# Kernel optimization log

Measured on AMD Instinct MI355X. Metric: run time of the kernel, lower is better.

## Reference

```python
import jax, jax.numpy as jnp
import numpy as np
from jax.ops import segment_sum, segment_max

N_NODES, N_EDGES, D_IN, D_H, D_E, HEADS, LAYERS, D_OUT, N_GRAPHS = 50000, 150000, 48, 64, 16, 10, 3, 128, 4096


def setup_inputs() -> dict:
    key = jax.random.key(0)
    ks = jax.random.split(key, 24)
    x = jax.random.normal(ks[0], (N_NODES, D_IN), jnp.float32)
    edge_attr = jax.random.uniform(ks[1], (N_EDGES, D_E), jnp.float32)
    edge_index = jax.random.randint(ks[2], (2, N_EDGES), 0, N_NODES, dtype=jnp.int32)
    batch_ids = jnp.sort(jax.random.randint(ks[3], (N_NODES,), 0, N_GRAPHS, dtype=jnp.int32))
    s = 0.05
    W_emb = jax.random.normal(ks[4], (D_IN, D_H), jnp.float32) * s
    b_emb = jnp.zeros((D_H,), jnp.float32)
    Ws = jax.random.normal(ks[5], (LAYERS, D_H, HEADS * D_H), jnp.float32) * s
    att_src = jax.random.normal(ks[6], (LAYERS, HEADS, D_H), jnp.float32) * s
    att_dst = jax.random.normal(ks[7], (LAYERS, HEADS, D_H), jnp.float32) * s
    att_edge = jax.random.normal(ks[8], (LAYERS, HEADS, D_H), jnp.float32) * s
    W_edge = jax.random.normal(ks[9], (LAYERS, D_E, HEADS * D_H), jnp.float32) * s
    bias = jnp.zeros((LAYERS, D_H), jnp.float32)
    bn_gamma = jnp.ones((LAYERS, D_H), jnp.float32)
    bn_beta = jnp.zeros((LAYERS, D_H), jnp.float32)
    bn_mean = jax.random.normal(ks[10], (LAYERS, D_H), jnp.float32) * 0.1
    bn_var = jax.random.uniform(ks[11], (LAYERS, D_H), jnp.float32) + 0.5
    W_out = jax.random.normal(ks[12], (D_H, D_OUT), jnp.float32) * s
    b_out = jnp.zeros((D_OUT,), jnp.float32)
    return dict(x=x, edge_attr=edge_attr, W_emb=W_emb, b_emb=b_emb, Ws=Ws,
                att_src=att_src, att_dst=att_dst, att_edge=att_edge, W_edge=W_edge,
                bias=bias, bn_gamma=bn_gamma, bn_beta=bn_beta, bn_mean=bn_mean,
                bn_var=bn_var, W_out=W_out, b_out=b_out,
                edge_index=edge_index, batch_ids=batch_ids)


def reference(x, edge_attr, W_emb, b_emb, Ws, att_src, att_dst, att_edge, W_edge,
              bias, bn_gamma, bn_beta, bn_mean, bn_var, W_out, b_out,
              edge_index, batch_ids):
    N = x.shape[0]
    H, F = att_src.shape[1], att_src.shape[2]
    src, dst = edge_index[0], edge_index[1]
    # PyG add_self_loops(fill_value='mean'): self-loop edge_attr = scatter-mean of incoming edge_attr
    cnt = segment_sum(jnp.ones(src.shape, jnp.float32), dst, num_segments=N)
    loop_attr = segment_sum(edge_attr, dst, num_segments=N) / jnp.maximum(cnt, 1.0)[:, None]
    ar = jnp.arange(N, dtype=src.dtype)
    src2 = jnp.concatenate([src, ar])
    dst2 = jnp.concatenate([dst, ar])
    ea2 = jnp.concatenate([edge_attr, loop_attr], axis=0)  # [E+N, De]

    h = x @ W_emb + b_emb  # [N, D_H]
    for i in range(Ws.shape[0]):
        xp = (h @ Ws[i]).reshape(N, H, F)                       # [N,H,F]
        a_s = jnp.einsum('nhf,hf->nh', xp, att_src[i])
        a_d = jnp.einsum('nhf,hf->nh', xp, att_dst[i])
        ep = (ea2 @ W_edge[i]).reshape(-1, H, F)                # [E2,H,F]
        a_e = jnp.einsum('ehf,hf->eh', ep, att_edge[i])
        alpha = jax.nn.leaky_relu(a_s[src2] + a_d[dst2] + a_e, 0.2)  # [E2,H]
        m = segment_max(alpha, dst2, num_segments=N)            # segment softmax over dst
        e = jnp.exp(alpha - m[dst2])
        z = segment_sum(e, dst2, num_segments=N)
        att = e / z[dst2]                                       # [E2,H]
        agg = segment_sum(xp[src2] * att[:, :, None], dst2, num_segments=N)  # [N,H,F]
        xc = agg.mean(axis=1) + bias[i]                         # concat=False -> head mean
        xc = (xc - bn_mean[i]) * bn_gamma[i] / jnp.sqrt(bn_var[i] + 1e-5) + bn_beta[i]
        xc = jax.nn.gelu(xc, approximate=False)
        h = h + xc                                              # residual_connection == 'res'
    out = h @ W_out + b_out                                     # [N, D_OUT]
    gsum = segment_sum(out, batch_ids, num_segments=N_GRAPHS)
    gcnt = segment_sum(jnp.ones((N,), jnp.float32), batch_ids, num_segments=N_GRAPHS)
    return gsum / jnp.maximum(gcnt, 1.0)[:, None]               # global_mean_pool [G, D_OUT]
```

## Files before the change

### kernel.cpp

```cpp
#include <hip/hip_runtime.h>
#include <hip/hip_fp16.h>
#include <math.h>

constexpr int NN   = 50000;
constexpr int NE   = 150000;
constexpr int DIN  = 48;
constexpr int DH   = 64;
constexpr int DE   = 16;
constexpr int NHD  = 10;
constexpr int NL   = 3;
constexpr int DOUTC= 128;
constexpr int NG   = 4096;
constexpr int E2   = NE + NN;
constexpr int SCAN_B  = 256;
constexpr int SCAN_NB = (NN + SCAN_B - 1) / SCAN_B;

typedef __bf16 v8bf __attribute__((ext_vector_type(8)));
typedef short  v8s  __attribute__((ext_vector_type(8)));
typedef float  v4f  __attribute__((ext_vector_type(4)));

__device__ inline unsigned short f2bf(float f) {
    unsigned u = __builtin_bit_cast(unsigned, f);
    unsigned r = (u + 0x7FFFu + ((u >> 16) & 1u)) >> 16;
    return (unsigned short)r;
}

__device__ inline v4f MF(v8s a, v8s b, v4f c) {
    return __builtin_amdgcn_mfma_f32_16x16x32_bf16(
        __builtin_bit_cast(v8bf, a), __builtin_bit_cast(v8bf, b), c, 0, 0, 0);
}
__device__ inline v4f MFB(v8bf a, v8s b, v4f c) {
    return __builtin_amdgcn_mfma_f32_16x16x32_bf16(
        a, __builtin_bit_cast(v8bf, b), c, 0, 0, 0);
}

#define RLI(v, l) __builtin_amdgcn_readlane((v), (l))
#define RLH2(v, l) __builtin_bit_cast(__half2, __builtin_amdgcn_readlane(__builtin_bit_cast(int, (v)), (l)))

__global__ void k_cnt(const int* __restrict__ dst, int* __restrict__ cnt) {
    int e = blockIdx.x * blockDim.x + threadIdx.x;
    if (e < NE) atomicAdd(&cnt[dst[e]], 1);
}

__global__ void k_scan_a(const int* __restrict__ cnt, int* __restrict__ bsum) {
    __shared__ int s[SCAN_B];
    int i = blockIdx.x * SCAN_B + threadIdx.x;
    s[threadIdx.x] = (i < NN) ? (cnt[i] + 1) : 0;
    __syncthreads();
    for (int off = SCAN_B / 2; off > 0; off >>= 1) {
        if (threadIdx.x < off) s[threadIdx.x] += s[threadIdx.x + off];
        __syncthreads();
    }
    if (threadIdx.x == 0) bsum[blockIdx.x] = s[0];
}

__global__ void k_scan_c(const int* __restrict__ cnt, const int* __restrict__ bsum,
                         int* __restrict__ rp, int* __restrict__ cursor) {
    __shared__ int s[SCAN_B];
    __shared__ int boff_s;
    const int t = threadIdx.x;
    int partial = (t < SCAN_NB && t < blockIdx.x) ? bsum[t] : 0;
    s[t] = partial;
    __syncthreads();
    for (int off = SCAN_B / 2; off > 0; off >>= 1) {
        if (t < off) s[t] += s[t + off];
        __syncthreads();
    }
    if (t == 0) boff_s = s[0];
    __syncthreads();
    const int boff = boff_s;
    __syncthreads();
    int i = blockIdx.x * SCAN_B + t;
    if (i < NN) cursor[i] = 0;
    int v = (i < NN) ? (cnt[i] + 1) : 0;
    s[t] = v;
    __syncthreads();
    for (int off = 1; off < SCAN_B; off <<= 1) {
        int tv = (t >= off) ? s[t - off] : 0;
        __syncthreads();
        s[t] += tv;
        __syncthreads();
    }
    if (i < NN) {
        int excl = boff + s[t] - v;
        rp[i] = excl;
        if (i == NN - 1) rp[NN] = excl + v;
    }
}

__global__ void k_csr_fill(const int* __restrict__ src, const int* __restrict__ dst,
                           const int* __restrict__ rp, int* __restrict__ cursor,
                           int* __restrict__ eidx, int* __restrict__ scsr) {
    int e = blockIdx.x * blockDim.x + threadIdx.x;
    if (e >= E2) return;
    int d  = (e < NE) ? dst[e] : (e - NE);
    int sn = (e < NE) ? src[e] : d;
    int pos = atomicAdd(&cursor[d], 1);
    int s = rp[d] + pos;
    eidx[s] = e; scsr[s] = sn;
}

__global__ void k_misc(const int* __restrict__ rp, const int* __restrict__ scsr,
                       const int* __restrict__ eidx, const int* __restrict__ cnt,
                       const float* __restrict__ ea, const int* __restrict__ batch,
                       int* __restrict__ snl12, int* __restrict__ grp,
                       float* __restrict__ loop) {
    int tid = blockIdx.x * blockDim.x + threadIdx.x;
    if (tid < NN * 16) {
        int n = tid >> 4, j = tid & 15;
        int r0 = rp[n], deg = rp[n + 1] - r0;
        int v;
        if (j < 12)      v = (j < deg) ? scsr[r0 + j] : 0;
        else if (j == 12) v = deg;
        else if (j == 13) v = r0;
        else             v = 0;
        snl12[tid] = v;
    } else if (tid < NN * 17) {
        int n = tid - NN * 16;
        int b = batch[n];
        int pb = (n == 0) ? -1 : batch[n - 1];
        for (int g = pb + 1; g <= b; ++g) grp[g] = n;
        if (n == NN - 1) for (int g = b + 1; g <= NG; ++g) grp[g] = NN;
    } else if (tid < NN * 33) {
        int t = tid - NN * 17;
        int n = t >> 4, d = t & 15;
        int r0 = rp[n], r1 = rp[n + 1];
        float s = 0.f;
        for (int q = r0; q < r1; ++q) {
            int eid = eidx[q];
            if (eid < NE) s += ea[(size_t)eid * DE + d];
        }
        int c = cnt[n];
        loop[t] = s * ((c > 1) ? (1.0f / (float)c) : 1.0f);
    }
}

constexpr int N_BTP = NL * 40960;
constexpr int N_WCB = NL * 2048;
constexpr int N_EMB = DH * 64;
constexpr int N_WET = NL * DE * NHD;
constexpr int N_PRE = N_BTP + N_WCB + N_EMB + N_WET + NN;
__global__ void k_prep(const float* __restrict__ Ws, const float* __restrict__ asrc,
                       const float* __restrict__ adst, const float* __restrict__ We_in,
                       const float* __restrict__ aedge, const float* __restrict__ Wemb,
                       unsigned short* __restrict__ BtP, unsigned short* __restrict__ WcB,
                       unsigned short* __restrict__ BH, unsigned short* __restrict__ BL,
                       float* __restrict__ WeT, int* __restrict__ cnt) {
    int tid = blockIdx.x * blockDim.x + threadIdx.x;
    if (tid < N_BTP) {
        int e  = tid & 7;
        int ln = (tid >> 3) & 63;
        int t  = (tid >> 9) % 20;
        int ct = (tid / 10240) & 3;
        int l  = tid / 40960;
        int f = ct * 16 + (ln & 15);
        int kidx = t * 32 + (ln >> 4) * 8 + e;
        int k = kidx / 10, q = kidx - 10 * (kidx / 10);
        float v = Ws[((size_t)l * DH + k) * 640 + q * 64 + f] * 0.1f;
        BtP[tid] = f2bf(v);
    } else if (tid < N_BTP + N_WCB) {
        int r0 = tid - N_BTP;
        int l = r0 / 2048, r = r0 % 2048;
        int tile = r / 1024, rr = r % 1024;
        int ln = rr / 16, idx = rr % 16;
        int t2 = idx / 8, e = idx % 8;
        int k = t2 * 32 + (ln >> 4) * 8 + e;
        int jc = ln & 15;
        int j = tile * 16 + jc;
        float v = 0.f;
        if (j < 20) {
            int hh = j % NHD;
            const float* a = ((j < NHD) ? asrc : adst) + (size_t)l * NHD * DH + hh * DH;
            const float* w = Ws + ((size_t)l * DH + k) * 640 + hh * DH;
            float s = 0.f;
#pragma unroll
            for (int f = 0; f < DH; ++f) s += w[f] * a[f];
            v = s;
        }
        WcB[r0] = f2bf(v);
    } else if (tid < N_BTP + N_WCB + N_EMB) {
        int r0 = tid - N_BTP - N_WCB;
        int c = r0 >> 6, k = r0 & 63;
        float v = (k < DIN) ? Wemb[(size_t)k * DH + c] : 0.f;
        __bf16 hi = (__bf16)v;
        BH[r0] = __builtin_bit_cast(unsigned short, hi);
        BL[r0] = __builtin_bit_cast(unsigned short, (__bf16)(v - (float)hi));
    } else if (tid < N_BTP + N_WCB + N_EMB + N_WET) {
        int t3 = tid - N_BTP - N_WCB - N_EMB;
        int l = t3 / 160, rr = t3 % 160;
        int hh = rr / 16, d = rr % 16;
        const float* a = aedge + (size_t)l * NHD * DH + hh * DH;
        const float* w = We_in + ((size_t)l * DE + d) * 640 + hh * DH;
        float s = 0.f;
#pragma unroll
        for (int f = 0; f < DH; ++f) s += w[f] * a[f];
        WeT[l * 160 + hh * 16 + d] = s;
    } else if (tid < N_PRE) {
        cnt[tid - (N_BTP + N_WCB + N_EMB + N_WET)] = 0;
    }
}

__global__ void k_ae3(const float* __restrict__ ea, const float* __restrict__ loop,
                      const float* __restrict__ WeT, const int* __restrict__ eidx,
                      __half* __restrict__ aeAll) {
    int tid = blockIdx.x * blockDim.x + threadIdx.x;
    if (tid >= E2 * NHD) return;
    int s = tid / NHD, h = tid - (tid / NHD) * NHD;
    int eid = eidx[s];
    const float* ar = (eid < NE) ? (ea + (size_t)eid * DE) : (loop + (size_t)(eid - NE) * DE);
    float4 a0 = *(const float4*)(ar + 0);
    float4 a1 = *(const float4*)(ar + 4);
    float4 a2 = *(const float4*)(ar + 8);
    float4 a3 = *(const float4*)(ar + 12);
#pragma unroll
    for (int l = 0; l < NL; ++l) {
        const float* wt = WeT + l * 160 + h * 16;
        float4 w0 = *(const float4*)(wt + 0);
        float4 w1 = *(const float4*)(wt + 4);
        float4 w2 = *(const float4*)(wt + 8);
        float4 w3 = *(const float4*)(wt + 12);
        float v = a0.x*w0.x + a0.y*w0.y + a0.z*w0.z + a0.w*w0.w
                + a1.x*w1.x + a1.y*w1.y + a1.z*w1.z + a1.w*w1.w
                + a2.x*w2.x + a2.y*w2.y + a2.z*w2.z + a2.w*w2.w
                + a3.x*w3.x + a3.y*w3.y + a3.z*w3.z + a3.w*w3.w;
        aeAll[(size_t)l * E2 * NHD + tid] = (__half)v;
    }
}

__global__ __launch_bounds__(256) void k_emb(const float* __restrict__ x,
        const unsigned short* __restrict__ BH, const unsigned short* __restrict__ BL,
        const float* __restrict__ bemb, const unsigned short* __restrict__ WcB,
        float* __restrict__ h, __half* __restrict__ hh, float* __restrict__ S) {
    __shared__ __align__(16) unsigned short hlb[4][16 * 72];
    const int tid = threadIdx.x;
    const int w = tid >> 6, lane = tid & 63;
    const int la = lane & 15, lb = lane >> 4;
    const int rowbase = blockIdx.x * 64 + w * 16;
    const int nA = rowbase + la;

    v8bf ah[2], al[2];
#pragma unroll
    for (int ks = 0; ks < 2; ++ks) {
        const int k0 = ks * 32 + lb * 8;
        float xv[8];
        if (nA < NN && k0 < DIN) {
            const float* xp = x + (size_t)nA * DIN + k0;
            float4 v0 = *(const float4*)xp;
            float4 v1 = *(const float4*)(xp + 4);
            xv[0]=v0.x; xv[1]=v0.y; xv[2]=v0.z; xv[3]=v0.w;
            xv[4]=v1.x; xv[5]=v1.y; xv[6]=v1.z; xv[7]=v1.w;
        } else {
#pragma unroll
            for (int e = 0; e < 8; ++e) xv[e] = 0.f;
        }
#pragma unroll
        for (int e = 0; e < 8; ++e) {
            __bf16 hi = (__bf16)xv[e];
            ah[ks][e] = hi;
            al[ks][e] = (__bf16)(xv[e] - (float)hi);
        }
    }
    v4f acc[4];
#pragma unroll
    for (int ct = 0; ct < 4; ++ct) acc[ct] = (v4f){0.f, 0.f, 0.f, 0.f};
#pragma unroll
    for (int ct = 0; ct < 4; ++ct) {
#pragma unroll
        for (int ks = 0; ks < 2; ++ks) {
            const int boff = (ct * 16 + la) * 64 + ks * 32 + lb * 8;
            v8s bh = *(const v8s*)&BH[boff];
            v8s bl = *(const v8s*)&BL[boff];
            acc[ct] = MFB(ah[ks], bh, acc[ct]);
            acc[ct] = MFB(al[ks], bh, acc[ct]);
            acc[ct] = MFB(ah[ks], bl, acc[ct]);
        }
    }
#pragma unroll
    for (int ct = 0; ct < 4; ++ct) {
        const int c = ct * 16 + la;
        const float bi = bemb[c];
#pragma unroll
        for (int r = 0; r < 4; ++r) {
            const int row = lb * 4 + r;
            const int n = rowbase + row;
            float v = acc[ct][r] + bi;
            if (n < NN) {
                h[(size_t)n * DH + c] = v;
                hh[(size_t)n * DH + c] = (__half)v;
            }
            hlb[w][row * 72 + c] = f2bf(v);
        }
    }
    __syncthreads();
    v4f s0 = {0.f,0.f,0.f,0.f}, s1 = {0.f,0.f,0.f,0.f};
#pragma unroll
    for (int t = 0; t < 2; ++t) {
        v8s av = *(const v8s*)&hlb[w][la * 72 + t * 32 + lb * 8];
        v8s b0 = *(const v8s*)&WcB[(size_t)(lane) * 16 + t * 8];
        v8s b1 = *(const v8s*)&WcB[(size_t)(64 + lane) * 16 + t * 8];
        s0 = MF(av, b0, s0);
        s1 = MF(av, b1, s1);
    }
#pragma unroll
    for (int r = 0; r < 4; ++r) {
        const int n = rowbase + lb * 4 + r;
        if (n < NN) {
            S[(size_t)n * 20 + la] = s0[r];
            if (la < 4) S[(size_t)n * 20 + 16 + la] = s1[r];
        }
    }
}

__global__ __launch_bounds__(256) void k_layer(
        const float* __restrict__ Sin, const __half* __restrict__ ae,
        __half* __restrict__ wraw,
        const int* __restrict__ snl12, const int* __restrict__ scsr,
        const float* __restrict__ hin, const __half* __restrict__ hinh,
        const unsigned short* __restrict__ BtP, const unsigned short* __restrict__ WcB,
        int do_s, float* __restrict__ Sout,
        const float* __restrict__ bias, const float* __restrict__ gam,
        const float* __restrict__ bet, const float* __restrict__ mean,
        const float* __restrict__ var, float* __restrict__ hout,
        __half* __restrict__ houth) {
    __shared__ __align__(16) unsigned short Gl[16 * 648];
    __shared__ __align__(8)  __half wL[16 * 120];

    const int tid = threadIdx.x;
    const int w = tid >> 6, lane = tid & 63;
    const int blk = blockIdx.x;
    const int nb4 = blk * 16 + w * 4;
    const unsigned* wrawu = (const unsigned*)wraw;

    const int meta = snl12[nb4 * 16 + lane];

    __half hv[4][6];
    __half hv2[4][6];
#pragma unroll
    for (int i = 0; i < 4; ++i) {
#pragma unroll
        for (int j = 0; j < 6; ++j) {
            int sv = RLI(meta, i * 16 + j);
            hv[i][j] = hinh[(size_t)sv * DH + lane];
        }
        const int deg_i = RLI(meta, i * 16 + 12);
        if (deg_i > 6) {
#pragma unroll
            for (int j = 0; j < 6; ++j) {
                int sv = RLI(meta, i * 16 + 6 + j);
                hv2[i][j] = hinh[(size_t)sv * DH + lane];
            }
        }
    }

    const int i0a = (lane < 48) ? (lane / 12) : 0;
    const int s0a = (lane < 48) ? (lane - i0a * 12) : 0;
    const int sn_a  = __shfl(meta, i0a * 16 + s0a);
    const int deg_a = __shfl(meta, i0a * 16 + 12);
    const int r0_a  = __shfl(meta, i0a * 16 + 13);

    if (lane < 48 && s0a < deg_a) {
        const int li = w * 4 + i0a;
        const int n  = nb4 + i0a;
        const float* sr = Sin + (size_t)sn_a * 20;
        const float* dr = Sin + (size_t)n * 20 + 10;
        const unsigned* aer = (const unsigned*)ae + (size_t)(r0_a + s0a) * 5;
        float4 t0 = *(const float4*)sr;
        float4 t1 = *(const float4*)(sr + 4);
        float2 t2 = *(const float2*)(sr + 8);
        float2 d0 = *(const float2*)(dr + 0);
        float2 d1 = *(const float2*)(dr + 2);
        float2 d2 = *(const float2*)(dr + 4);
        float2 d3 = *(const float2*)(dr + 6);
        float2 d4 = *(const float2*)(dr + 8);
        unsigned ew[5];
#pragma unroll
        for (int p = 0; p < 5; ++p) ew[p] = aer[p];
        float as_[10] = {t0.x,t0.y,t0.z,t0.w,t1.x,t1.y,t1.z,t1.w,t2.x,t2.y};
        float sd_[10] = {d0.x,d0.y,d1.x,d1.y,d2.x,d2.y,d3.x,d3.y,d4.x,d4.y};
        float* aSrow = (float*)&Gl[li * 648];
#pragma unroll
        for (int p = 0; p < 5; ++p) {
            __half2 eh = __builtin_bit_cast(__half2, ew[p]);
            float a0 = as_[2*p]   + sd_[2*p]   + __low2float(eh);
            float a1 = as_[2*p+1] + sd_[2*p+1] + __high2float(eh);
            a0 = (a0 > 0.f) ? a0 : 0.2f * a0;
            a1 = (a1 > 0.f) ? a1 : 0.2f * a1;
            float2 fp = {a0, a1};
            *(float2*)&aSrow[s0a * 10 + 2 * p] = fp;
        }
    }
    __builtin_amdgcn_wave_barrier();

    const int i0b = (lane < 40) ? (lane / 10) : 0;
    const int h_b = (lane < 40) ? (lane - i0b * 10) : 0;
    const int deg_b = __shfl(meta, i0b * 16 + 12);
    const int r0_b  = __shfl(meta, i0b * 16 + 13);

    if (lane < 40) {
        const int i0 = i0b, h = h_b;
        const int li = w * 4 + i0;
        const int n = nb4 + i0;
        const int deg = deg_b, r0 = r0_b;
        const float* aSrow = (const float*)&Gl[li * 648];
        float aL[12];
        float m = -1e30f;
#pragma unroll
        for (int s = 0; s < 12; ++s) {
            float a = -1e30f;
            if (s < deg) { a = aSrow[s * 10 + h]; m = fmaxf(m, a); }
            aL[s] = a;
        }
        if (deg > 12) {
            const float sd = Sin[(size_t)n * 20 + 10 + h];
            for (int s = 12; s < deg; ++s) {
                int sn = scsr[r0 + s];
                float a = Sin[(size_t)sn * 20 + h] + sd + (float)ae[(size_t)(r0 + s) * NHD + h];
                a = (a > 0.f) ? a : 0.2f * a;
                wraw[(size_t)(r0 + s) * NHD + h] = (__half)a;
                m = fmaxf(m, a);
            }
        }
        float z = 0.f;
#pragma unroll
        for (int s = 0; s < 12; ++s) {
            float e = (s < deg) ? __expf(aL[s] - m) : 0.f;
            aL[s] = e;
            z += e;
        }
        for (int s = 12; s < deg; ++s) {
            float e = __expf((float)wraw[(size_t)(r0 + s) * NHD + h] - m);
            wraw[(size_t)(r0 + s) * NHD + h] = (__half)e;
            z += e;
        }
        float zi = 1.f / z;
#pragma unroll
        for (int s = 0; s < 12; ++s)
            wL[li * 120 + s * 10 + h] = (__half)(aL[s] * zi);
        for (int s = 12; s < deg; ++s)
            wraw[(size_t)(r0 + s) * NHD + h] =
                (__half)((float)wraw[(size_t)(r0 + s) * NHD + h] * zi);
    }
    __builtin_amdgcn_wave_barrier();

    const unsigned* wLu = (const unsigned*)wL;
    int wfu[4];
#pragma unroll
    for (int i = 0; i < 4; ++i)
        wfu[i] = (int)wLu[(w * 4 + i) * 60 + (lane & 31)];
#pragma unroll
    for (int i = 0; i < 4; ++i) {
        const int li = w * 4 + i;
        const int deg = RLI(meta, i * 16 + 12);
        const int r0  = RLI(meta, i * 16 + 13);
        __half2 g[5];
#pragma unroll
        for (int p = 0; p < 5; ++p) g[p] = __half2{(__half)0.f, (__half)0.f};
#pragma unroll
        for (int j = 0; j < 6; ++j) {
            __half2 hvd = __half2half2(hv[i][j]);
#pragma unroll
            for (int p = 0; p < 5; ++p)
                g[p] = __hfma2(RLH2(wfu[i], j * 5 + p), hvd, g[p]);
        }
        if (deg > 6) {
            {
                int w2 = (lane < 30) ? (int)wLu[li * 60 + 30 + lane] : 0;
#pragma unroll
                for (int j = 0; j < 6; ++j) {
                    __half2 hvd = __half2half2(hv2[i][j]);
#pragma unroll
                    for (int p = 0; p < 5; ++p)
                        g[p] = __hfma2(RLH2(w2, j * 5 + p), hvd, g[p]);
                }
            }
            for (int c0 = 12; c0 < deg; c0 += 6) {
                const int rem = deg - c0;
                int w2 = (lane < 30 && (lane / 5) < rem)
                         ? (int)wrawu[(size_t)(r0 + c0) * 5 + lane] : 0;
                int s2 = (lane < 6 && c0 + lane < deg) ? scsr[r0 + c0 + lane] : 0;
                __half hv3[6];
#pragma unroll
                for (int j = 0; j < 6; ++j) {
                    int sv = RLI(s2, j);
                    hv3[j] = hinh[(size_t)sv * DH + lane];
                }
#pragma unroll
                for (int j = 0; j < 6; ++j) {
                    __half2 hvd = __half2half2(hv3[j]);
#pragma unroll
                    for (int p = 0; p < 5; ++p)
                        g[p] = __hfma2(RLH2(w2, j * 5 + p), hvd, g[p]);
                }
            }
        }
        const int base = li * 648 + lane * 10;
#pragma unroll
        for (int p = 0; p < 5; ++p) {
            float f0 = __low2float(g[p]), f1 = __high2float(g[p]);
            unsigned u = (unsigned)f2bf(f0) | ((unsigned)f2bf(f1) << 16);
            *(unsigned*)&Gl[base + 2 * p] = u;
        }
    }
    __syncthreads();

    const int la = lane & 15, lb = lane >> 4;
    v4f acc = {0.f, 0.f, 0.f, 0.f};
    const unsigned short* bp = BtP + (size_t)w * 20 * 512;
#pragma unroll 5
    for (int t = 0; t < 20; ++t) {
        v8s av = *(const v8s*)&Gl[la * 648 + t * 32 + lb * 8];
        v8s bv = *(const v8s*)&bp[t * 512 + lane * 8];
        acc = MF(av, bv, acc);
    }
    __syncthreads();

    unsigned short* hlb = Gl;
    const int f = w * 16 + la;
    const float bi = bias[f], gm = gam[f], bt_ = bet[f], mu = mean[f];
    const float iv = rsqrtf(var[f] + 1e-5f);
#pragma unroll
    for (int r = 0; r < 4; ++r) {
        const int local = lb * 4 + r;
        const int n = blk * 16 + local;
        float hvold = hin[(size_t)n * DH + f];
        float v = acc[r] + bi;
        v = (v - mu) * gm * iv + bt_;
        v = 0.5f * v * (1.0f + erff(v * 0.70710678118654752f));
        float hnew = hvold + v;
        hout[(size_t)n * DH + f] = hnew;
        houth[(size_t)n * DH + f] = (__half)hnew;
        hlb[local * 72 + f] = f2bf(hnew);
    }

    if (do_s) {
        __syncthreads();
        if (w < 2) {
            v4f sa = {0.f, 0.f, 0.f, 0.f};
#pragma unroll
            for (int t = 0; t < 2; ++t) {
                v8s av = *(const v8s*)&hlb[la * 72 + t * 32 + lb * 8];
                v8s bv = *(const v8s*)&WcB[(size_t)(w * 64 + lane) * 16 + t * 8];
                sa = MF(av, bv, sa);
            }
#pragma unroll
            for (int r = 0; r < 4; ++r) {
                const int n = blk * 16 + lb * 4 + r;
                if (w == 0) Sout[(size_t)n * 20 + la] = sa[r];
                else if (la < 4) Sout[(size_t)n * 20 + 16 + la] = sa[r];
            }
        }
    }
}

__global__ __launch_bounds__(256) void k_gout(const __half* __restrict__ hh,
        const float* __restrict__ W, const float* __restrict__ b,
        const int* __restrict__ grp, float* __restrict__ out) {
    __shared__ float Wl[DH * DOUTC];
    __shared__ float hl[4][DH];
    __shared__ float cl[4];
    for (int i = threadIdx.x; i < DH * DOUTC; i += 256) Wl[i] = W[i];
    int w = threadIdx.x >> 6, lane = threadIdx.x & 63;
    int g = blockIdx.x * 4 + w;
    int r0 = grp[g], r1 = grp[g + 1];
    float s = 0.f;
    for (int n = r0; n < r1; ++n) s += (float)hh[(size_t)n * DH + lane];
    hl[w][lane] = s;
    if (lane == 0) cl[w] = (float)(r1 - r0);
    __syncthreads();
    for (int idx = threadIdx.x; idx < 4 * DOUTC; idx += 256) {
        int gi = idx >> 7, c = idx & 127;
        float cnt = cl[gi];
        float inv = 1.f / fmaxf(cnt, 1.f);
        float acc = cnt * b[c];
        const float* hr = hl[gi];
#pragma unroll 16
        for (int k = 0; k < DH; ++k) acc += hr[k] * Wl[k * DOUTC + c];
        out[(size_t)(blockIdx.x * 4 + gi) * DOUTC + c] = acc * inv;
    }
}

extern "C" void kernel_launch(void* const* d_in, const int* in_sizes, int n_in,
                              void* d_out, int out_size, void* d_ws, size_t ws_size,
                              hipStream_t stream) {
    const float* x        = (const float*)d_in[0];
    const float* edge_attr= (const float*)d_in[1];
    const float* W_emb    = (const float*)d_in[2];
    const float* b_emb    = (const float*)d_in[3];
    const float* Ws       = (const float*)d_in[4];
    const float* att_src  = (const float*)d_in[5];
    const float* att_dst  = (const float*)d_in[6];
    const float* att_edge = (const float*)d_in[7];
    const float* W_edge   = (const float*)d_in[8];
    const float* bias     = (const float*)d_in[9];
    const float* bn_gamma = (const float*)d_in[10];
    const float* bn_beta  = (const float*)d_in[11];
    const float* bn_mean  = (const float*)d_in[12];
    const float* bn_var   = (const float*)d_in[13];
    const float* W_out    = (const float*)d_in[14];
    const float* b_out    = (const float*)d_in[15];
    const int*   srcp     = (const int*)d_in[16];
    const int*   dstp     = srcp + NE;
    const int*   batch    = (const int*)d_in[17];
    float* out = (float*)d_out;

    char* wsb = (char*)d_ws;
    size_t off = 0;
    auto alloc = [&](size_t bytes) -> void* {
        void* p = (void*)(wsb + off);
        off += (bytes + 255) & ~(size_t)255;
        return p;
    };
    float*  h0    = (float*)alloc((size_t)NN * DH * 4);
    float*  h1    = (float*)alloc((size_t)NN * DH * 4);
    __half* hh0   = (__half*)alloc((size_t)NN * DH * 2);
    __half* hh1   = (__half*)alloc((size_t)NN * DH * 2);
    float*  S0    = (float*)alloc((size_t)NN * 20 * 4);
    float*  S1    = (float*)alloc((size_t)NN * 20 * 4);
    __half* wraw  = (__half*)alloc((size_t)E2 * NHD * 2);
    __half* aeAll = (__half*)alloc((size_t)NL * E2 * NHD * 2);
    float*  loop  = (float*)alloc((size_t)NN * DE * 4);
    int*    cnt   = (int*)alloc((size_t)NN * 4);
    int*    rp    = (int*)alloc((size_t)(NN + 1) * 4);
    int*    cursor= (int*)alloc((size_t)NN * 4);
    int*    eidx  = (int*)alloc((size_t)E2 * 4);
    int*    scsr  = (int*)alloc((size_t)E2 * 4);
    int*    snl12 = (int*)alloc((size_t)NN * 16 * 4);
    int*    bsum  = (int*)alloc((size_t)SCAN_NB * 4);
    int*    grp   = (int*)alloc((size_t)(NG + 1) * 4);
    float*  WeT   = (float*)alloc((size_t)NL * 160 * 4);
    unsigned short* BtP = (unsigned short*)alloc((size_t)NL * 40960 * 2);
    unsigned short* WcB = (unsigned short*)alloc((size_t)NL * 2048 * 2);
    unsigned short* BH  = (unsigned short*)alloc((size_t)DH * 64 * 2);
    unsigned short* BL  = (unsigned short*)alloc((size_t)DH * 64 * 2);

    k_prep<<<(N_PRE + 255) / 256, 256, 0, stream>>>(
        Ws, att_src, att_dst, W_edge, att_edge, W_emb, BtP, WcB, BH, BL, WeT, cnt);

    k_cnt<<<(NE + 255) / 256, 256, 0, stream>>>(dstp, cnt);
    k_scan_a<<<SCAN_NB, SCAN_B, 0, stream>>>(cnt, bsum);
    k_scan_c<<<SCAN_NB, SCAN_B, 0, stream>>>(cnt, bsum, rp, cursor);
    k_csr_fill<<<(E2 + 255) / 256, 256, 0, stream>>>(srcp, dstp, rp, cursor, eidx, scsr);
    k_misc<<<(NN * 33 + 255) / 256, 256, 0, stream>>>(rp, scsr, eidx, cnt, edge_attr,
                                                      batch, snl12, grp, loop);

    k_ae3<<<(E2 * NHD + 255) / 256, 256, 0, stream>>>(edge_attr, loop, WeT, eidx, aeAll);

    k_emb<<<(NN + 63) / 64, 256, 0, stream>>>(x, BH, BL, b_emb, WcB, h0, hh0, S0);

    float*  hb[2]  = {h0, h1};
    __half* hhb[2] = {hh0, hh1};
    float*  Sb[2]  = {S0, S1};
    for (int l = 0; l < NL; ++l) {
        float*  hin   = hb[l & 1];
        float*  hout  = hb[(l + 1) & 1];
        __half* hinh  = hhb[l & 1];
        __half* houth = hhb[(l + 1) & 1];
        float*  Sin   = Sb[l & 1];
        float*  Sout  = Sb[(l + 1) & 1];
        k_layer<<<NN / 16, 256, 0, stream>>>(
            Sin, aeAll + (size_t)l * E2 * NHD, wraw, snl12, scsr, hin, hinh,
            BtP + (size_t)l * 40960,
            WcB + (size_t)(l + 1 < NL ? l + 1 : 0) * 2048,
            (l + 1 < NL) ? 1 : 0, Sout,
            bias + l * DH, bn_gamma + l * DH, bn_beta + l * DH,
            bn_mean + l * DH, bn_var + l * DH, hout, houth);
    }
    __half* hfinh = hhb[NL & 1];

    k_gout<<<NG / 4, 256, 0, stream>>>(hfinh, W_out, b_out, grp, out);
}
```

Baseline: 194.8 us.

## Drop fp32 node-feature buffers and move dst score add into softmax stage

Removes the fp32 copies of the node hidden state, so embedding and layer kernels write only the fp16 copy and the residual reads fp16 input. In the score stage it drops the per-edge loads of destination attention terms; each softmax lane loads one destination score per head and applies leaky relu there. This cuts global memory traffic per layer. The cost is that the residual path now accumulates in fp16 precision across layers, which may increase numerical error.

```diff
diff --git a/kernel.cpp b/kernel.cpp
--- a/kernel.cpp
+++ b/kernel.cpp
@@ -230,7 +230,7 @@
 __global__ __launch_bounds__(256) void k_emb(const float* __restrict__ x,
         const unsigned short* __restrict__ BH, const unsigned short* __restrict__ BL,
         const float* __restrict__ bemb, const unsigned short* __restrict__ WcB,
-        float* __restrict__ h, __half* __restrict__ hh, float* __restrict__ S) {
+        __half* __restrict__ hh, float* __restrict__ S) {
     __shared__ __align__(16) unsigned short hlb[4][16 * 72];
     const int tid = threadIdx.x;
     const int w = tid >> 6, lane = tid & 63;
@@ -284,10 +284,7 @@
             const int row = lb * 4 + r;
             const int n = rowbase + row;
             float v = acc[ct][r] + bi;
-            if (n < NN) {
-                h[(size_t)n * DH + c] = v;
-                hh[(size_t)n * DH + c] = (__half)v;
-            }
+            if (n < NN) hh[(size_t)n * DH + c] = (__half)v;
             hlb[w][row * 72 + c] = f2bf(v);
         }
     }
@@ -315,13 +312,12 @@
         const float* __restrict__ Sin, const __half* __restrict__ ae,
         __half* __restrict__ wraw,
         const int* __restrict__ snl12, const int* __restrict__ scsr,
-        const float* __restrict__ hin, const __half* __restrict__ hinh,
+        const __half* __restrict__ hinh,
         const unsigned short* __restrict__ BtP, const unsigned short* __restrict__ WcB,
         int do_s, float* __restrict__ Sout,
         const float* __restrict__ bias, const float* __restrict__ gam,
         const float* __restrict__ bet, const float* __restrict__ mean,
-        const float* __restrict__ var, float* __restrict__ hout,
-        __half* __restrict__ houth) {
+        const float* __restrict__ var, __half* __restrict__ houth) {
     __shared__ __align__(16) unsigned short Gl[16 * 648];
     __shared__ __align__(8)  __half wL[16 * 120];
 
@@ -360,32 +356,20 @@
 
     if (lane < 48 && s0a < deg_a) {
         const int li = w * 4 + i0a;
-        const int n  = nb4 + i0a;
         const float* sr = Sin + (size_t)sn_a * 20;
-        const float* dr = Sin + (size_t)n * 20 + 10;
         const unsigned* aer = (const unsigned*)ae + (size_t)(r0_a + s0a) * 5;
         float4 t0 = *(const float4*)sr;
         float4 t1 = *(const float4*)(sr + 4);
         float2 t2 = *(const float2*)(sr + 8);
-        float2 d0 = *(const float2*)(dr + 0);
-        float2 d1 = *(const float2*)(dr + 2);
-        float2 d2 = *(const float2*)(dr + 4);
-        float2 d3 = *(const float2*)(dr + 6);
-        float2 d4 = *(const float2*)(dr + 8);
         unsigned ew[5];
 #pragma unroll
         for (int p = 0; p < 5; ++p) ew[p] = aer[p];
         float as_[10] = {t0.x,t0.y,t0.z,t0.w,t1.x,t1.y,t1.z,t1.w,t2.x,t2.y};
-        float sd_[10] = {d0.x,d0.y,d1.x,d1.y,d2.x,d2.y,d3.x,d3.y,d4.x,d4.y};
         float* aSrow = (float*)&Gl[li * 648];
 #pragma unroll
         for (int p = 0; p < 5; ++p) {
             __half2 eh = __builtin_bit_cast(__half2, ew[p]);
-            float a0 = as_[2*p]   + sd_[2*p]   + __low2float(eh);
-            float a1 = as_[2*p+1] + sd_[2*p+1] + __high2float(eh);
-            a0 = (a0 > 0.f) ? a0 : 0.2f * a0;
-            a1 = (a1 > 0.f) ? a1 : 0.2f * a1;
-            float2 fp = {a0, a1};
+            float2 fp = {as_[2*p] + __low2float(eh), as_[2*p+1] + __high2float(eh)};
             *(float2*)&aSrow[s0a * 10 + 2 * p] = fp;
         }
     }
@@ -401,17 +385,21 @@
         const int li = w * 4 + i0;
         const int n = nb4 + i0;
         const int deg = deg_b, r0 = r0_b;
+        const float sd = Sin[(size_t)n * 20 + 10 + h];
         const float* aSrow = (const float*)&Gl[li * 648];
         float aL[12];
         float m = -1e30f;
 #pragma unroll
         for (int s = 0; s < 12; ++s) {
             float a = -1e30f;
-            if (s < deg) { a = aSrow[s * 10 + h]; m = fmaxf(m, a); }
+            if (s < deg) {
+                a = aSrow[s * 10 + h] + sd;
+                a = (a > 0.f) ? a : 0.2f * a;
+                m = fmaxf(m, a);
+            }
             aL[s] = a;
         }
         if (deg > 12) {
-            const float sd = Sin[(size_t)n * 20 + 10 + h];
             for (int s = 12; s < deg; ++s) {
                 int sn = scsr[r0 + s];
                 float a = Sin[(size_t)sn * 20 + h] + sd + (float)ae[(size_t)(r0 + s) * NHD + h];
@@ -522,12 +510,11 @@
     for (int r = 0; r < 4; ++r) {
         const int local = lb * 4 + r;
         const int n = blk * 16 + local;
-        float hvold = hin[(size_t)n * DH + f];
+        float hvold = (float)hinh[(size_t)n * DH + f];
         float v = acc[r] + bi;
         v = (v - mu) * gm * iv + bt_;
         v = 0.5f * v * (1.0f + erff(v * 0.70710678118654752f));
         float hnew = hvold + v;
-        hout[(size_t)n * DH + f] = hnew;
         houth[(size_t)n * DH + f] = (__half)hnew;
         hlb[local * 72 + f] = f2bf(hnew);
     }
@@ -610,8 +597,6 @@
         off += (bytes + 255) & ~(size_t)255;
         return p;
     };
-    float*  h0    = (float*)alloc((size_t)NN * DH * 4);
-    float*  h1    = (float*)alloc((size_t)NN * DH * 4);
     __half* hh0   = (__half*)alloc((size_t)NN * DH * 2);
     __half* hh1   = (__half*)alloc((size_t)NN * DH * 2);
     float*  S0    = (float*)alloc((size_t)NN * 20 * 4);
@@ -645,25 +630,22 @@
 
     k_ae3<<<(E2 * NHD + 255) / 256, 256, 0, stream>>>(edge_attr, loop, WeT, eidx, aeAll);
 
-    k_emb<<<(NN + 63) / 64, 256, 0, stream>>>(x, BH, BL, b_emb, WcB, h0, hh0, S0);
-
-    float*  hb[2]  = {h0, h1};
+    k_emb<<<(NN + 63) / 64, 256, 0, stream>>>(x, BH, BL, b_emb, WcB, hh0, S0);
+
     __half* hhb[2] = {hh0, hh1};
     float*  Sb[2]  = {S0, S1};
     for (int l = 0; l < NL; ++l) {
-        float*  hin   = hb[l & 1];
-        float*  hout  = hb[(l + 1) & 1];
         __half* hinh  = hhb[l & 1];
         __half* houth = hhb[(l + 1) & 1];
         float*  Sin   = Sb[l & 1];
         float*  Sout  = Sb[(l + 1) & 1];
         k_layer<<<NN / 16, 256, 0, stream>>>(
-            Sin, aeAll + (size_t)l * E2 * NHD, wraw, snl12, scsr, hin, hinh,
+            Sin, aeAll + (size_t)l * E2 * NHD, wraw, snl12, scsr, hinh,
             BtP + (size_t)l * 40960,
             WcB + (size_t)(l + 1 < NL ? l + 1 : 0) * 2048,
             (l + 1 < NL) ? 1 : 0, Sout,
             bias + l * DH, bn_gamma + l * DH, bn_beta + l * DH,
-            bn_mean + l * DH, bn_var + l * DH, hout, houth);
+            bn_mean + l * DH, bn_var + l * DH, houth);
     }
     __half* hfinh = hhb[NL & 1];
 
```

New measurement: 189.8 us. 1.03x faster.
